# Optimization experiments

Hardware: AMD Instinct MI355X
Metric: run time of the kernel (lower is better)

Reference implementation:

```python
import jax, jax.numpy as jnp
import numpy as np

N, E = 50000, 1600000
IN, OUT, H = 128, 32, 2
NT, ET = 20, 4
ETE, EAE, ED = 16, 16, 16
SLOPE = 0.2  # conv_neg_slope


def setup_inputs() -> dict:
    key = jax.random.key(0)
    ks = jax.random.split(key, 11)
    d_att = 2 * OUT + ETE + EAE
    return dict(
        x=jax.random.normal(ks[0], (N, IN), jnp.float32),
        edge_index=jax.random.randint(ks[1], (2, E), 0, N),
        ntypes=jax.random.randint(ks[2], (N,), 0, NT),
        etypes=jax.random.randint(ks[3], (E,), 0, ET),
        eattr=jax.random.normal(ks[4], (E, ED), jnp.float32),
        het_W=jax.random.normal(ks[5], (NT, IN, OUT), jnp.float32) / np.sqrt(IN).astype(np.float32),
        het_b=jnp.zeros((NT, OUT), jnp.float32),
        etype_table=jax.random.normal(ks[6], (ET, ETE), jnp.float32),
        eattr_W=jax.random.normal(ks[7], (ED, EAE), jnp.float32) / np.sqrt(ED).astype(np.float32),
        att_W=jax.random.normal(ks[8], (d_att, H), jnp.float32) / np.sqrt(d_att).astype(np.float32),
        lin_W=jax.random.normal(ks[9], (OUT + EAE, OUT), jnp.float32) / np.sqrt(OUT + EAE).astype(np.float32),
    )


def _lrelu(v):
    return jax.nn.leaky_relu(v, SLOPE)


def _heat_conv(x, edge_index, ntypes, etypes, eattr,
               het_W, het_b, etype_table, eattr_W, att_W, lin_W):
    # HeteroLinear: node-type-conditioned linear transform (loop over 20 types,
    # avoids materializing a [N, IN, OUT] gathered-weight tensor)
    h = jnp.zeros((x.shape[0], het_W.shape[-1]), x.dtype)
    for t in range(het_W.shape[0]):
        h = h + jnp.where((ntypes == t)[:, None], x @ het_W[t] + het_b[t], 0.0)

    src, dst = edge_index[0], edge_index[1]
    ete = _lrelu(etype_table[etypes])        # [E, ETE] edge-type embedding
    ea = _lrelu(eattr @ eattr_W)             # [E, EAE] edge-attr embedding
    x_i = h[dst]                             # target node feats [E, OUT]
    x_j = h[src]                             # source node feats [E, OUT]

    feat = jnp.concatenate([x_i, x_j, ete, ea], axis=-1)
    alpha = _lrelu(feat @ att_W)             # [E, H] raw attention logits

    # softmax grouped by destination node, per head
    amax = jax.ops.segment_max(alpha, dst, num_segments=N)  # [N, H]
    alpha = jnp.exp(alpha - amax[dst])
    denom = jax.ops.segment_sum(alpha, dst, num_segments=N)  # [N, H]
    alpha = alpha / denom[dst]

    msg = jnp.concatenate([x_j, ea], axis=-1) @ lin_W        # [E, OUT]
    m = (msg[:, None, :] * alpha[:, :, None]).reshape(alpha.shape[0], H * OUT)
    out = jax.ops.segment_sum(m, dst, num_segments=N)        # [N, H*OUT]
    return out  # concat=True -> flattened heads


def reference(x, edge_index, ntypes, etypes, eattr,
              het_W, het_b, etype_table, eattr_W, att_W, lin_W):
    out = _heat_conv(x, edge_index, ntypes, etypes, eattr,
                     het_W, het_b, etype_table, eattr_W, att_W, lin_W)
    return jax.nn.relu(out)  # final activation in forward (eval mode: no dropout)
```

## Files before the change

### kernel.cpp

```cpp
#include <hip/hip_runtime.h>
#include <hip/hip_fp16.h>

#define NN 50000
#define EE 1600000
#define IN_F 128
#define SLOPE 0.2f
#define NB_SCAN 196
#define NPAD 16

typedef _Float16 hf2 __attribute__((ext_vector_type(2)));

__global__ __launch_bounds__(256) void k_node(
    const float* __restrict__ x, const int* __restrict__ ntypes,
    const float* __restrict__ hetW, const float* __restrict__ hetb,
    const float* __restrict__ linW, const float* __restrict__ attW,
    float* __restrict__ hlin, float* __restrict__ auxS,
    float* __restrict__ auxD)
{
    __shared__ float sH[32 * 33];
    __shared__ float sLin[32 * 32];
    int tid = threadIdx.x;
    for (int i = tid; i < 1024; i += 256) sLin[i] = linW[i];

    int g = tid >> 3;
    int j = tid & 7;
    int n = blockIdx.x * 32 + g;
    int nc = n < NN ? n : NN - 1;
    int t = ntypes[nc];
    const float* W = hetW + (size_t)t * (IN_F * 32);
    const float4* xr = (const float4*)(x + (size_t)nc * IN_F);

    float4 acc = ((const float4*)(hetb + t * 32))[j];
    #pragma unroll 4
    for (int c = 0; c < 32; ++c) {
        float4 xv = xr[c];
        const float* Wr = W + (4 * c) * 32 + 4 * j;
        float4 w0 = *(const float4*)(Wr);
        float4 w1 = *(const float4*)(Wr + 32);
        float4 w2 = *(const float4*)(Wr + 64);
        float4 w3 = *(const float4*)(Wr + 96);
        acc.x += xv.x * w0.x + xv.y * w1.x + xv.z * w2.x + xv.w * w3.x;
        acc.y += xv.x * w0.y + xv.y * w1.y + xv.z * w2.y + xv.w * w3.y;
        acc.z += xv.x * w0.z + xv.y * w1.z + xv.z * w2.z + xv.w * w3.z;
        acc.w += xv.x * w0.w + xv.y * w1.w + xv.z * w2.w + xv.w * w3.w;
    }
    sH[g * 33 + 4 * j + 0] = acc.x;
    sH[g * 33 + 4 * j + 1] = acc.y;
    sH[g * 33 + 4 * j + 2] = acc.z;
    sH[g * 33 + 4 * j + 3] = acc.w;
    __syncthreads();

    int o = tid & 31;
    #pragma unroll
    for (int pass = 0; pass < 4; ++pass) {
        int g2 = (tid >> 5) + 8 * pass;
        int n2 = blockIdx.x * 32 + g2;
        if (n2 >= NN) break;
        float accl = 0.0f;
        #pragma unroll
        for (int k = 0; k < 32; ++k)
            accl += sH[g2 * 33 + k] * sLin[k * 32 + o];
        hlin[(size_t)n2 * 32 + o] = accl;

        float hv = sH[g2 * 33 + o];
        float p0 = hv * attW[o * 2],        p1 = hv * attW[o * 2 + 1];
        float p2 = hv * attW[(32 + o) * 2], p3 = hv * attW[(32 + o) * 2 + 1];
        #pragma unroll
        for (int m = 16; m >= 1; m >>= 1) {
            p0 += __shfl_xor(p0, m, 32);
            p1 += __shfl_xor(p1, m, 32);
            p2 += __shfl_xor(p2, m, 32);
            p3 += __shfl_xor(p3, m, 32);
        }
        if (o == 0) {
            auxD[n2 * 2] = p0; auxD[n2 * 2 + 1] = p1;
            auxS[n2 * 2] = p2; auxS[n2 * 2 + 1] = p3;
        }
    }
}

__global__ __launch_bounds__(256) void k_count(
    const int* __restrict__ dst, int* __restrict__ count)
{
    int e = blockIdx.x * 256 + threadIdx.x;
    atomicAdd(&count[dst[e]], 1);
}

__global__ __launch_bounds__(256) void k_scanA(
    const int* __restrict__ count, int* __restrict__ offsets,
    int* __restrict__ bsum)
{
    __shared__ int s[256];
    int t = threadIdx.x;
    int i = blockIdx.x * 256 + t;
    int c = (i < NN) ? count[i] : 0;
    s[t] = c;
    __syncthreads();
    for (int off = 1; off < 256; off <<= 1) {
        int v = (t >= off) ? s[t - off] : 0;
        __syncthreads();
        s[t] += v;
        __syncthreads();
    }
    if (i < NN) offsets[i] = s[t] - c;
    if (t == 255) bsum[blockIdx.x] = s[255];
}

__global__ __launch_bounds__(256) void k_scanB(
    const int* __restrict__ bsum, int* __restrict__ bbase,
    const float* __restrict__ etab, const float* __restrict__ attW,
    float* __restrict__ etedot)
{
    __shared__ int s[256];
    int t = threadIdx.x;
    if (t < 8) {
        int et = t >> 1, hh = t & 1;
        float acc = 0.0f;
        for (int k = 0; k < 16; ++k) {
            float v = etab[et * 16 + k];
            v = v > 0.0f ? v : SLOPE * v;
            acc += v * attW[(64 + k) * 2 + hh];
        }
        etedot[t] = acc;
    }
    int c = (t < NB_SCAN) ? bsum[t] : 0;
    s[t] = c;
    __syncthreads();
    for (int off = 1; off < 256; off <<= 1) {
        int v = (t >= off) ? s[t - off] : 0;
        __syncthreads();
        s[t] += v;
        __syncthreads();
    }
    if (t < NB_SCAN) bbase[t] = s[t] - c;
}

__global__ __launch_bounds__(256) void k_scanC(
    int* __restrict__ offsets, const int* __restrict__ bbase,
    int* __restrict__ nextPad)
{
    int t = threadIdx.x;
    int i = blockIdx.x * 256 + t;
    if (i < NN) {
        int v = offsets[i] + bbase[blockIdx.x];
        offsets[i] = v;
        nextPad[i * NPAD] = v;
    }
    if (i == 0) offsets[NN] = EE;
}

__global__ __launch_bounds__(256) void k_pre5(
    const int* __restrict__ srcp, const int* __restrict__ dstp,
    const int* __restrict__ etypes, const float* __restrict__ eattr,
    const float* __restrict__ eaW, const float* __restrict__ attW,
    const float* __restrict__ etedot, const float* __restrict__ auxS,
    const float* __restrict__ auxD, int* __restrict__ nextPad,
    float4* __restrict__ recBuf)
{
    int e = blockIdx.x * 256 + threadIdx.x;
    int s = srcp[e], d = dstp[e], et = etypes[e];
    int slot = atomicAdd(&nextPad[d * NPAD], 1);

    float attr[16];
    {
        const float4* ap = (const float4*)(eattr + (size_t)e * 16);
        #pragma unroll
        for (int q = 0; q < 4; ++q) {
            float4 v = ap[q];
            attr[4*q+0] = v.x; attr[4*q+1] = v.y;
            attr[4*q+2] = v.z; attr[4*q+3] = v.w;
        }
    }
    float ea[16];
    #pragma unroll
    for (int j = 0; j < 16; ++j) {
        float acc = 0.0f;
        #pragma unroll
        for (int k = 0; k < 16; ++k) acc += attr[k] * eaW[k * 16 + j];
        ea[j] = acc > 0.0f ? acc : SLOPE * acc;
    }

    float2 aD = ((const float2*)auxD)[d];
    float2 aS = ((const float2*)auxS)[s];
    float2 eD = ((const float2*)etedot)[et];
    float al0 = aD.x + aS.x + eD.x;
    float al1 = aD.y + aS.y + eD.y;
    #pragma unroll
    for (int j = 0; j < 16; ++j) {
        al0 += ea[j] * attW[(80 + j) * 2];
        al1 += ea[j] * attW[(80 + j) * 2 + 1];
    }
    al0 = al0 > 0.0f ? al0 : SLOPE * al0;
    al1 = al1 > 0.0f ? al1 : SLOPE * al1;
    float p0 = __expf(al0), p1 = __expf(al1);

    __half2 eh[8];
    #pragma unroll
    for (int q = 0; q < 8; ++q)
        eh[q] = __floats2half2_rn(ea[2*q], ea[2*q+1]);

    float4* P = recBuf + (size_t)slot * 4;
    P[0] = ((const float4*)eh)[0];
    P[1] = ((const float4*)eh)[1];
    union { float4 v; int i[4]; float f[4]; } mu;
    mu.i[0] = s; mu.f[1] = p0; mu.f[2] = p1; mu.i[3] = 0;
    P[2] = mu.v;
    P[3] = make_float4(0.f, 0.f, 0.f, 0.f);
}

__global__ __launch_bounds__(256) void k_gather5(
    const int* __restrict__ offsets, const float4* __restrict__ recBuf,
    const float* __restrict__ hlin, const float* __restrict__ linW,
    float* __restrict__ out)
{
    int tid = blockIdx.x * 256 + threadIdx.x;
    int n = tid >> 6;
    int lane = threadIdx.x & 63;
    if (n >= NN) return;
    int o = lane & 31, hh = lane >> 5, j = o & 15;

    int s0 = __builtin_amdgcn_readfirstlane(offsets[n]);
    int s1 = __builtin_amdgcn_readfirstlane(offsets[n + 1]);

    const char* base = (const char*)recBuf;
    float accm = 0.0f, accp = 0.0f, wacc = 0.0f;

    int slot = s0;
    for (; slot + 3 < s1; slot += 4) {
        const char* r0 = base + ((size_t)(slot + 0) << 6);
        const char* r1 = base + ((size_t)(slot + 1) << 6);
        const char* r2 = base + ((size_t)(slot + 2) << 6);
        const char* r3 = base + ((size_t)(slot + 3) << 6);
        int4 m0 = *(const int4*)(r0 + 32);
        int4 m1 = *(const int4*)(r1 + 32);
        int4 m2 = *(const int4*)(r2 + 32);
        int4 m3 = *(const int4*)(r3 + 32);
        float e0 = __half2float(*(const __half*)(r0 + 2 * j));
        float e1 = __half2float(*(const __half*)(r1 + 2 * j));
        float e2 = __half2float(*(const __half*)(r2 + 2 * j));
        float e3 = __half2float(*(const __half*)(r3 + 2 * j));
        float hv0 = hlin[(size_t)m0.x * 32 + o];
        float hv1 = hlin[(size_t)m1.x * 32 + o];
        float hv2 = hlin[(size_t)m2.x * 32 + o];
        float hv3 = hlin[(size_t)m3.x * 32 + o];
        float p0 = __int_as_float(hh ? m0.z : m0.y);
        float p1 = __int_as_float(hh ? m1.z : m1.y);
        float p2 = __int_as_float(hh ? m2.z : m2.y);
        float p3 = __int_as_float(hh ? m3.z : m3.y);
        accm += p0 * hv0;
        accm += p1 * hv1;
        accm += p2 * hv2;
        accm += p3 * hv3;
        wacc += p0 * e0;
        wacc += p1 * e1;
        wacc += p2 * e2;
        wacc += p3 * e3;
        accp += (p0 + p1) + (p2 + p3);
    }
    for (; slot < s1; ++slot) {
        const char* r = base + ((size_t)slot << 6);
        int4 m = *(const int4*)(r + 32);
        float e = __half2float(*(const __half*)(r + 2 * j));
        float hv = hlin[(size_t)m.x * 32 + o];
        float p = __int_as_float(hh ? m.z : m.y);
        accm += p * hv;
        wacc += p * e;
        accp += p;
    }

    float elin = 0.0f;
    int bsel = lane & 32;
    #pragma unroll
    for (int jj = 0; jj < 16; ++jj) {
        float wv = __shfl(wacc, bsel | jj, 64);
        elin += wv * linW[(32 + jj) * 32 + o];
    }
    float num = accm + elin;
    float v = accp > 0.0f ? num / accp : 0.0f;
    out[(size_t)n * 64 + lane] = v > 0.0f ? v : 0.0f;
}

extern "C" void kernel_launch(void* const* d_in, const int* in_sizes, int n_in,
                              void* d_out, int out_size, void* d_ws, size_t ws_size,
                              hipStream_t stream)
{
    const float* x      = (const float*)d_in[0];
    const int*   eidx   = (const int*)  d_in[1];
    const int*   ntypes = (const int*)  d_in[2];
    const int*   etypes = (const int*)  d_in[3];
    const float* eattr  = (const float*)d_in[4];
    const float* hetW   = (const float*)d_in[5];
    const float* hetb   = (const float*)d_in[6];
    const float* etab   = (const float*)d_in[7];
    const float* eaW    = (const float*)d_in[8];
    const float* attW   = (const float*)d_in[9];
    const float* linW   = (const float*)d_in[10];
    float* out = (float*)d_out;

    char* ws = (char*)d_ws;
    size_t off = 0;
    auto alloc = [&](size_t bytes) {
        char* p = ws + off;
        off = (off + bytes + 255) & ~(size_t)255;
        return p;
    };
    float*  hlin     = (float*) alloc((size_t)NN * 32 * sizeof(float));
    float*  auxS     = (float*) alloc((size_t)NN * 2 * sizeof(float));
    float*  auxD     = (float*) alloc((size_t)NN * 2 * sizeof(float));
    float*  etedot   = (float*) alloc(8 * sizeof(float));
    int*    count    = (int*)   alloc((size_t)NN * sizeof(int));
    int*    offsets  = (int*)   alloc(((size_t)NN + 1) * sizeof(int));
    int*    nextPad  = (int*)   alloc((size_t)NN * NPAD * sizeof(int));
    int*    bsum     = (int*)   alloc(256 * sizeof(int));
    int*    bbase    = (int*)   alloc(256 * sizeof(int));
    float4* recBuf   = (float4*)alloc((size_t)EE * 64);
    (void)ws_size;

    const int* srcp = eidx;
    const int* dstp = eidx + EE;

    hipMemsetAsync(count, 0, (size_t)NN * sizeof(int), stream);

    k_node<<<(NN + 31) / 32, 256, 0, stream>>>(x, ntypes, hetW, hetb, linW,
                                               attW, hlin, auxS, auxD);
    k_count<<<EE / 256, 256, 0, stream>>>(dstp, count);
    k_scanA<<<NB_SCAN, 256, 0, stream>>>(count, offsets, bsum);
    k_scanB<<<1, 256, 0, stream>>>(bsum, bbase, etab, attW, etedot);
    k_scanC<<<NB_SCAN, 256, 0, stream>>>(offsets, bbase, nextPad);
    k_pre5<<<EE / 256, 256, 0, stream>>>(srcp, dstp, etypes, eattr, eaW, attW,
                                         etedot, auxS, auxD, nextPad, recBuf);
    k_gather5<<<(NN * 64 + 255) / 256, 256, 0, stream>>>(offsets, recBuf,
                                                         hlin, linW, out);
}
```

Before: 496.3 us.

## Shard destination counts per XCC and reuse count-atomic ranks for CSR slots

```diff
diff --git a/kernel.cpp b/kernel.cpp
--- a/kernel.cpp
+++ b/kernel.cpp
@@ -6,7 +6,7 @@
 #define IN_F 128
 #define SLOPE 0.2f
 #define NB_SCAN 196
-#define NPAD 16
+#define NSHARD 8
 
 typedef _Float16 hf2 __attribute__((ext_vector_type(2)));
 
@@ -80,21 +80,37 @@
 }
 
 __global__ __launch_bounds__(256) void k_count(
-    const int* __restrict__ dst, int* __restrict__ count)
+    const int* __restrict__ dst, int* __restrict__ cnt8,
+    unsigned* __restrict__ rankpack)
 {
     int e = blockIdx.x * 256 + threadIdx.x;
-    atomicAdd(&count[dst[e]], 1);
+    int d = dst[e];
+    unsigned xcc;
+    asm volatile("s_getreg_b32 %0, hwreg(HW_REG_XCC_ID)" : "=s"(xcc));
+    int sh = xcc & (NSHARD - 1);
+    int lr = atomicAdd(&cnt8[sh * NN + d], 1);
+    rankpack[e] = ((unsigned)lr << 3) | (unsigned)sh;
 }
 
 __global__ __launch_bounds__(256) void k_scanA(
-    const int* __restrict__ count, int* __restrict__ offsets,
-    int* __restrict__ bsum)
+    const int* __restrict__ cnt8, int* __restrict__ offsets,
+    int* __restrict__ bsum, int* __restrict__ sb8)
 {
     __shared__ int s[256];
     int t = threadIdx.x;
     int i = blockIdx.x * 256 + t;
-    int c = (i < NN) ? count[i] : 0;
-    s[t] = c;
+    int tot = 0;
+    if (i < NN) {
+        int pre = 0;
+        #pragma unroll
+        for (int sh = 0; sh < NSHARD; ++sh) {
+            int c = cnt8[sh * NN + i];
+            sb8[sh * NN + i] = pre;
+            pre += c;
+        }
+        tot = pre;
+    }
+    s[t] = tot;
     __syncthreads();
     for (int off = 1; off < 256; off <<= 1) {
         int v = (t >= off) ? s[t - off] : 0;
@@ -102,7 +118,7 @@
         s[t] += v;
         __syncthreads();
     }
-    if (i < NN) offsets[i] = s[t] - c;
+    if (i < NN) offsets[i] = s[t] - tot;
     if (t == 255) bsum[blockIdx.x] = s[255];
 }
 
@@ -137,29 +153,32 @@
 
 __global__ __launch_bounds__(256) void k_scanC(
     int* __restrict__ offsets, const int* __restrict__ bbase,
-    int* __restrict__ nextPad)
+    int* __restrict__ sb8)
 {
     int t = threadIdx.x;
     int i = blockIdx.x * 256 + t;
     if (i < NN) {
         int v = offsets[i] + bbase[blockIdx.x];
         offsets[i] = v;
-        nextPad[i * NPAD] = v;
+        #pragma unroll
+        for (int sh = 0; sh < NSHARD; ++sh)
+            sb8[sh * NN + i] += v;
     }
     if (i == 0) offsets[NN] = EE;
 }
 
-__global__ __launch_bounds__(256) void k_pre5(
+__global__ __launch_bounds__(256) void k_pre6(
     const int* __restrict__ srcp, const int* __restrict__ dstp,
     const int* __restrict__ etypes, const float* __restrict__ eattr,
     const float* __restrict__ eaW, const float* __restrict__ attW,
     const float* __restrict__ etedot, const float* __restrict__ auxS,
-    const float* __restrict__ auxD, int* __restrict__ nextPad,
-    float4* __restrict__ recBuf)
+    const float* __restrict__ auxD, const unsigned* __restrict__ rankpack,
+    const int* __restrict__ sb8, float4* __restrict__ recBuf)
 {
     int e = blockIdx.x * 256 + threadIdx.x;
     int s = srcp[e], d = dstp[e], et = etypes[e];
-    int slot = atomicAdd(&nextPad[d * NPAD], 1);
+    unsigned rp = rankpack[e];
+    int slot = sb8[(size_t)(rp & 7) * NN + d] + (int)(rp >> 3);
 
     float attr[16];
     {
@@ -304,31 +323,33 @@
         off = (off + bytes + 255) & ~(size_t)255;
         return p;
     };
-    float*  hlin     = (float*) alloc((size_t)NN * 32 * sizeof(float));
-    float*  auxS     = (float*) alloc((size_t)NN * 2 * sizeof(float));
-    float*  auxD     = (float*) alloc((size_t)NN * 2 * sizeof(float));
-    float*  etedot   = (float*) alloc(8 * sizeof(float));
-    int*    count    = (int*)   alloc((size_t)NN * sizeof(int));
-    int*    offsets  = (int*)   alloc(((size_t)NN + 1) * sizeof(int));
-    int*    nextPad  = (int*)   alloc((size_t)NN * NPAD * sizeof(int));
-    int*    bsum     = (int*)   alloc(256 * sizeof(int));
-    int*    bbase    = (int*)   alloc(256 * sizeof(int));
-    float4* recBuf   = (float4*)alloc((size_t)EE * 64);
+    float*    hlin     = (float*)   alloc((size_t)NN * 32 * sizeof(float));
+    float*    auxS     = (float*)   alloc((size_t)NN * 2 * sizeof(float));
+    float*    auxD     = (float*)   alloc((size_t)NN * 2 * sizeof(float));
+    float*    etedot   = (float*)   alloc(8 * sizeof(float));
+    int*      cnt8     = (int*)     alloc((size_t)NSHARD * NN * sizeof(int));
+    int*      offsets  = (int*)     alloc(((size_t)NN + 1) * sizeof(int));
+    int*      sb8      = (int*)     alloc((size_t)NSHARD * NN * sizeof(int));
+    unsigned* rankpack = (unsigned*)alloc((size_t)EE * sizeof(unsigned));
+    int*      bsum     = (int*)     alloc(256 * sizeof(int));
+    int*      bbase    = (int*)     alloc(256 * sizeof(int));
+    float4*   recBuf   = (float4*)  alloc((size_t)EE * 64);
     (void)ws_size;
 
     const int* srcp = eidx;
     const int* dstp = eidx + EE;
 
-    hipMemsetAsync(count, 0, (size_t)NN * sizeof(int), stream);
+    hipMemsetAsync(cnt8, 0, (size_t)NSHARD * NN * sizeof(int), stream);
 
     k_node<<<(NN + 31) / 32, 256, 0, stream>>>(x, ntypes, hetW, hetb, linW,
                                                attW, hlin, auxS, auxD);
-    k_count<<<EE / 256, 256, 0, stream>>>(dstp, count);
-    k_scanA<<<NB_SCAN, 256, 0, stream>>>(count, offsets, bsum);
+    k_count<<<EE / 256, 256, 0, stream>>>(dstp, cnt8, rankpack);
+    k_scanA<<<NB_SCAN, 256, 0, stream>>>(cnt8, offsets, bsum, sb8);
     k_scanB<<<1, 256, 0, stream>>>(bsum, bbase, etab, attW, etedot);
-    k_scanC<<<NB_SCAN, 256, 0, stream>>>(offsets, bbase, nextPad);
-    k_pre5<<<EE / 256, 256, 0, stream>>>(srcp, dstp, etypes, eattr, eaW, attW,
-                                         etedot, auxS, auxD, nextPad, recBuf);
+    k_scanC<<<NB_SCAN, 256, 0, stream>>>(offsets, bbase, sb8);
+    k_pre6<<<EE / 256, 256, 0, stream>>>(srcp, dstp, etypes, eattr, eaW, attW,
+                                         etedot, auxS, auxD, rankpack, sb8,
+                                         recBuf);
     k_gather5<<<(NN * 64 + 255) / 256, 256, 0, stream>>>(offsets, recBuf,
                                                          hlin, linW, out);
 }
```

Result: faster. 464.6 us (-6.4%).
